# Performance work log

Hardware: AMD Instinct MI355X
Metric: run time of the kernel (lower is better)

Reference implementation:

```python
import jax, jax.numpy as jnp
import numpy as np

SPATIAL_SHAPES = [(128, 128), (64, 64), (32, 32), (16, 16)]  # sum HW = 21760
N_HEADS, N_LEVELS, N_POINTS, EMBED = 8, 4, 4, 256
HEAD_D = EMBED // N_HEADS
B, NQ = 2, 10000
NV = sum(h * w for h, w in SPATIAL_SHAPES)


def setup_inputs() -> dict:
    key = jax.random.key(0)
    ks = jax.random.split(key, 12)
    s = 0.02
    return {
        "query": jax.random.normal(ks[0], (B, NQ, EMBED), jnp.float32),
        "key": jax.random.normal(ks[1], (B, NV, EMBED), jnp.float32),
        "value": jax.random.normal(ks[2], (B, NV, EMBED), jnp.float32),
        "W_off": jax.random.normal(ks[3], (EMBED, N_HEADS * N_LEVELS * N_POINTS * 2), jnp.float32) * s,
        "b_off": jax.random.uniform(ks[4], (N_HEADS * N_LEVELS * N_POINTS * 2,), jnp.float32, -0.9, 0.9),
        "W_attn": jax.random.normal(ks[5], (EMBED, N_HEADS * N_LEVELS * N_POINTS), jnp.float32) * s,
        "b_attn": jnp.zeros((N_HEADS * N_LEVELS * N_POINTS,), jnp.float32),
        "W_v": jax.random.normal(ks[6], (EMBED, EMBED), jnp.float32) * s,
        "b_v": jnp.zeros((EMBED,), jnp.float32),
        "W_out": jax.random.normal(ks[7], (EMBED, EMBED), jnp.float32) * s,
        "b_out": jnp.zeros((EMBED,), jnp.float32),
    }


def bilinear_sample(img, gx, gy):
    """img: [N, Hs, Ws, C]; gx, gy: [N, P] in [-1, 1].
    Torch grid_sample semantics: bilinear, align_corners=True, padding_mode='zeros'.
    gx indexes width, gy indexes height."""
    N, Hs, Ws, C = img.shape
    px = (gx + 1.0) * 0.5 * (Ws - 1)
    py = (gy + 1.0) * 0.5 * (Hs - 1)
    x0 = jnp.floor(px)
    y0 = jnp.floor(py)
    wx = (px - x0)[..., None]
    wy = (py - y0)[..., None]
    x0i = x0.astype(jnp.int32)
    y0i = y0.astype(jnp.int32)
    flat = img.reshape(N, Hs * Ws, C)

    def gather(xi, yi):
        valid = ((xi >= 0) & (xi < Ws) & (yi >= 0) & (yi < Hs))[..., None]
        xc = jnp.clip(xi, 0, Ws - 1)
        yc = jnp.clip(yi, 0, Hs - 1)
        idx = yc * Ws + xc  # [N, P]
        v = jnp.take_along_axis(flat, idx[..., None], axis=1)  # [N, P, C]
        return jnp.where(valid, v, 0.0)

    v00 = gather(x0i, y0i)
    v01 = gather(x0i + 1, y0i)
    v10 = gather(x0i, y0i + 1)
    v11 = gather(x0i + 1, y0i + 1)
    top = v00 * (1.0 - wx) + v01 * wx
    bot = v10 * (1.0 - wx) + v11 * wx
    return top * (1.0 - wy) + bot * wy


def reference(query, key, value, W_off, b_off, W_attn, b_attn, W_v, b_v, W_out, b_out):
    Bq, Nq, _ = query.shape
    # value projection -> per-head values
    v = (value @ W_v + b_v).reshape(Bq, NV, N_HEADS, HEAD_D)
    # sampling locations (used directly as normalized [-1,1] grid coords) and weights
    off = (query @ W_off + b_off).reshape(Bq, Nq, N_HEADS, N_LEVELS, N_POINTS, 2)
    attn = (query @ W_attn + b_attn).reshape(Bq, Nq, N_HEADS, N_LEVELS, N_POINTS)
    attn = jax.nn.softmax(attn, axis=-1)  # softmax over points per level (as in source)

    out = jnp.zeros((Bq, Nq, EMBED), query.dtype)
    start = 0
    for lvl, (Hs, Ws) in enumerate(SPATIAL_SHAPES):
        vl = v[:, start:start + Hs * Ws].reshape(Bq, Hs, Ws, N_HEADS, HEAD_D)
        start += Hs * Ws
        vl = vl.transpose(0, 3, 1, 2, 4).reshape(Bq * N_HEADS, Hs, Ws, HEAD_D)
        gl = off[:, :, :, lvl]  # [B, Nq, H, P, 2]
        gl = gl.transpose(0, 2, 1, 3, 4).reshape(Bq * N_HEADS, Nq * N_POINTS, 2)
        samp = bilinear_sample(vl, gl[..., 0], gl[..., 1])  # [B*H, Nq*P, D]
        samp = samp.reshape(Bq, N_HEADS, Nq, N_POINTS, HEAD_D)
        wl = attn[:, :, :, lvl].transpose(0, 2, 1, 3)  # [B, H, Nq, P]
        out = out + jnp.einsum('bhqp,bhqpd->bqhd', wl, samp).reshape(Bq, Nq, EMBED)
    return out @ W_out + b_out
```

## Files before the change

### kernel.cpp

```cpp
#include <hip/hip_runtime.h>
#include <math.h>

#define B_   2
#define NQ_  10000
#define NV_  21760
#define EMB  256
#define MQ   (B_*NQ_)
#define MV   (B_*NV_)

typedef short bf16x8 __attribute__((ext_vector_type(8)));
typedef float f32x4  __attribute__((ext_vector_type(4)));

__device__ constexpr int LSc[4] = {0, 16384, 20480, 21504};

__device__ __forceinline__ unsigned short f2bf(float x) {
  unsigned u = __builtin_bit_cast(unsigned, x);
  u += 0x7FFFu + ((u >> 16) & 1u);
  return (unsigned short)(u >> 16);
}
__device__ __forceinline__ float bf2f(unsigned short s) {
  return __builtin_bit_cast(float, (unsigned)s << 16);
}

__global__ __launch_bounds__(256) void prep_weights(
    const float* __restrict__ Wv, const float* __restrict__ Wattn,
    const float* __restrict__ Woff, const float* __restrict__ Wout,
    unsigned short* __restrict__ WvT, unsigned short* __restrict__ WoutT,
    unsigned short* __restrict__ WqHi, unsigned short* __restrict__ WqLo) {
  int n = blockIdx.x;
  int k = threadIdx.x;
  if (n < 256) {
    WvT[n * 256 + k] = f2bf(Wv[k * 256 + n]);
  } else if (n < 512) {
    int c = n - 256;
    WoutT[c * 256 + k] = f2bf(Wout[k * 256 + c]);
  } else {
    int qr = n - 512;
    float x = (qr < 256) ? Woff[k * 256 + qr] : Wattn[k * 128 + (qr - 256)];
    unsigned short hi = f2bf(x);
    WqHi[qr * 256 + k] = hi;
    WqLo[qr * 256 + k] = f2bf(x - bf2f(hi));
  }
}

template <int MODE, typename OutT, bool VPERM = false>
__global__ __launch_bounds__(256) void gemm_mfma(
    const void* __restrict__ Aa,
    const unsigned short* __restrict__ Bt, const unsigned short* __restrict__ Bt2,
    const float* __restrict__ bias, const float* __restrict__ bias2,
    OutT* __restrict__ C, float* __restrict__ C2, int M, int N) {
  constexpr int BM = 128, BK = 32;
  __shared__ unsigned short As[(MODE == 3 ? 2 : 1) * BM * BK];
  __shared__ unsigned short Bs[(MODE == 3 ? 2 : 1) * BM * BK];
  unsigned short* As2 = As + BM * BK;
  unsigned short* Bs2 = Bs + BM * BK;

  const int tid = threadIdx.x;
  const int lane = tid & 63, wv = tid >> 6;
  const int wr = wv >> 1, wc = wv & 1;
  const int row0 = blockIdx.x * BM, col0 = blockIdx.y * BM;

  auto lds_addr = [](int row, int kslot) -> int {
    return row * 64 + ((kslot ^ ((row >> 1) & 3)) << 4);
  };

  auto stage_bf = [&](unsigned short* dst, const unsigned short* src,
                      int rbase, int rmax, int kk) {
#pragma unroll
    for (int i = 0; i < 2; ++i) {
      int idx = tid + 256 * i;
      int row = idx >> 2, ks = idx & 3;
      int rg = min(rbase + row, rmax);
      bf16x8 vdat = *(const bf16x8*)(src + (size_t)rg * 256 + kk + ks * 8);
      *(bf16x8*)((char*)dst + lds_addr(row, ks)) = vdat;
    }
  };
  auto stage_cvt = [&](unsigned short* dst, const float* src,
                       int rbase, int rmax, int kk) {
#pragma unroll
    for (int i = 0; i < 4; ++i) {
      int idx = tid + 256 * i;
      int row = idx >> 3, c4 = idx & 7;
      int rg = min(rbase + row, rmax);
      float4 vdat = *(const float4*)(src + (size_t)rg * 256 + kk + c4 * 4);
      ushort4 o;
      o.x = f2bf(vdat.x); o.y = f2bf(vdat.y);
      o.z = f2bf(vdat.z); o.w = f2bf(vdat.w);
      *(ushort4*)((char*)dst + lds_addr(row, c4 >> 1) + (c4 & 1) * 8) = o;
    }
  };
  auto stage_cvt2 = [&](unsigned short* dstH, unsigned short* dstL,
                        const float* src, int rbase, int rmax, int kk) {
#pragma unroll
    for (int i = 0; i < 4; ++i) {
      int idx = tid + 256 * i;
      int row = idx >> 3, c4 = idx & 7;
      int rg = min(rbase + row, rmax);
      float4 vdat = *(const float4*)(src + (size_t)rg * 256 + kk + c4 * 4);
      ushort4 hh, ll;
      hh.x = f2bf(vdat.x); ll.x = f2bf(vdat.x - bf2f(hh.x));
      hh.y = f2bf(vdat.y); ll.y = f2bf(vdat.y - bf2f(hh.y));
      hh.z = f2bf(vdat.z); ll.z = f2bf(vdat.z - bf2f(hh.z));
      hh.w = f2bf(vdat.w); ll.w = f2bf(vdat.w - bf2f(hh.w));
      int a = lds_addr(row, c4 >> 1) + (c4 & 1) * 8;
      *(ushort4*)((char*)dstH + a) = hh;
      *(ushort4*)((char*)dstL + a) = ll;
    }
  };

  const bool three_term = (MODE == 3) && (col0 < 256);

  f32x4 acc[4][4] = {};

  for (int kk = 0; kk < 256; kk += BK) {
    if (kk) __syncthreads();
    if constexpr (MODE == 1)
      stage_cvt(As, (const float*)Aa, row0, M - 1, kk);
    else if constexpr (MODE == 3) {
      if (three_term)
        stage_cvt2(As, As2, (const float*)Aa, row0, M - 1, kk);
      else
        stage_cvt(As, (const float*)Aa, row0, M - 1, kk);
    } else
      stage_bf(As, (const unsigned short*)Aa, row0, M - 1, kk);
    stage_bf(Bs, Bt, col0, N - 1, kk);
    if constexpr (MODE == 3)
      if (three_term) stage_bf(Bs2, Bt2, col0, N - 1, kk);
    __syncthreads();

    const int kslot = lane >> 4;
    bf16x8 af[4], bfr[4];
#pragma unroll
    for (int i = 0; i < 4; ++i) {
      int ra = wr * 64 + i * 16 + (lane & 15);
      af[i] = *(const bf16x8*)((const char*)As + lds_addr(ra, kslot));
      int rb = wc * 64 + i * 16 + (lane & 15);
      bfr[i] = *(const bf16x8*)((const char*)Bs + lds_addr(rb, kslot));
    }
#pragma unroll
    for (int mi = 0; mi < 4; ++mi)
#pragma unroll
      for (int ni = 0; ni < 4; ++ni)
        acc[mi][ni] = __builtin_amdgcn_mfma_f32_16x16x32_bf16(
            af[mi], bfr[ni], acc[mi][ni], 0, 0, 0);

    if constexpr (MODE == 3) {
      if (three_term) {
        bf16x8 af2[4], bfr2[4];
#pragma unroll
        for (int i = 0; i < 4; ++i) {
          int ra = wr * 64 + i * 16 + (lane & 15);
          af2[i] = *(const bf16x8*)((const char*)As2 + lds_addr(ra, kslot));
          int rb = wc * 64 + i * 16 + (lane & 15);
          bfr2[i] = *(const bf16x8*)((const char*)Bs2 + lds_addr(rb, kslot));
        }
#pragma unroll
        for (int mi = 0; mi < 4; ++mi)
#pragma unroll
          for (int ni = 0; ni < 4; ++ni) {
            acc[mi][ni] = __builtin_amdgcn_mfma_f32_16x16x32_bf16(
                af2[mi], bfr[ni], acc[mi][ni], 0, 0, 0);
            acc[mi][ni] = __builtin_amdgcn_mfma_f32_16x16x32_bf16(
                af[mi], bfr2[ni], acc[mi][ni], 0, 0, 0);
          }
      }
    }
  }

  if constexpr (VPERM) {
    float bb4[4];
#pragma unroll
    for (int ni = 0; ni < 4; ++ni)
      bb4[ni] = bias[col0 + wc * 64 + ni * 16 + (lane & 15)];
#pragma unroll
    for (int mi = 0; mi < 4; ++mi) {
#pragma unroll
      for (int r = 0; r < 4; ++r) {
        int row = row0 + wr * 64 + mi * 16 + ((lane >> 4) << 2) + r;
        int pix = row, bb2 = 0;
        if (pix >= NV_) { bb2 = 1; pix -= NV_; }
        int lvl = (pix >= 16384) + (pix >= 20480) + (pix >= 21504);
        int sh = 7 - lvl;
        int rel = pix - LSc[lvl];
        int x = rel & ((1 << sh) - 1), y = rel >> sh;
        unsigned pairoff = ((unsigned)((y << (sh - 1)) + (x >> 1)) << 10) |
                           ((unsigned)(x & 1) << 3);
        char* vout = (char*)C + ((size_t)bb2 * NV_ + LSc[lvl]) * 512 + pairoff;
#pragma unroll
        for (int ni = 0; ni < 4; ++ni) {
          int gcol = col0 + wc * 64 + ni * 16 + (lane & 15);
          float val = acc[mi][ni][r] + bb4[ni];
          int h = gcol >> 5, d = gcol & 31;
          *(unsigned short*)(vout + h * 128 + (d >> 2) * 16 + (d & 3) * 2) =
              f2bf(val);
        }
      }
    }
  } else {
#pragma unroll
    for (int ni = 0; ni < 4; ++ni) {
      int gcol = col0 + wc * 64 + ni * 16 + (lane & 15);
      float bb = (MODE == 3 && gcol >= 256) ? bias2[gcol - 256] : bias[gcol];
#pragma unroll
      for (int mi = 0; mi < 4; ++mi) {
        int rowbase = row0 + wr * 64 + mi * 16 + ((lane >> 4) << 2);
        f32x4 a = acc[mi][ni];
#pragma unroll
        for (int r = 0; r < 4; ++r) {
          int row = rowbase + r;
          if (row < M) {
            float val = a[r] + bb;
            if constexpr (MODE == 3) {
              if (gcol >= 256)
                C2[(size_t)row * 128 + (gcol - 256)] = val;
              else
                C[(size_t)row * 256 + gcol] = (OutT)val;
            } else if constexpr (sizeof(OutT) == 2) {
              C[(size_t)row * N + gcol] = (OutT)f2bf(val);
            } else {
              C[(size_t)row * N + gcol] = (OutT)val;
            }
          }
        }
      }
    }
  }
}

__global__ __launch_bounds__(256) void msda_sample6(
    const char* __restrict__ v,
    const float* __restrict__ off,
    const float* __restrict__ attnlg,
    ushort4* __restrict__ tmp4) {
  __shared__ unsigned coeff[4 * 136 * 8];
  const int lane = threadIdx.x & 63;
  const int wq = threadIdx.x >> 6;
  const int bq = blockIdx.x * 4 + wq;
  const int b = (blockIdx.x * 4) / NQ_;

  unsigned* cbase = coeff + wq * (136 * 8);
  const float* offq = off + (size_t)bq * 256;
  const float* attq = attnlg + (size_t)bq * 128;

#pragma unroll
  for (int i = 0; i < 2; ++i) {
    int c = lane + i * 64;
    int h = c >> 4, l = (c >> 2) & 3, p = c & 3;
    int Wl = 128 >> l, sh = 7 - l;

    const float* lg = attq + h * 16 + l * 4;
    float l0 = lg[0], l1 = lg[1], l2 = lg[2], l3 = lg[3];
    float m = fmaxf(fmaxf(l0, l1), fmaxf(l2, l3));
    float e0 = expf(l0 - m), e1 = expf(l1 - m);
    float e2 = expf(l2 - m), e3 = expf(l3 - m);
    float ep = (p == 0) ? e0 : (p == 1) ? e1 : (p == 2) ? e2 : e3;
    float wsm = ep / (e0 + e1 + e2 + e3);

    float gx = offq[h * 32 + (l * 4 + p) * 2 + 0];
    float gy = offq[h * 32 + (l * 4 + p) * 2 + 1];
    float s = 0.5f * (float)(Wl - 1);
    float px = fmaf(gx, s, s), py = fmaf(gy, s, s);
    float x0f = floorf(px), y0f = floorf(py);
    float wx = px - x0f, wy = py - y0f;
    int x0 = (int)x0f, y0 = (int)y0f;

    bool bx0 = (unsigned)x0 < (unsigned)Wl, bx1 = (unsigned)(x0 + 1) < (unsigned)Wl;
    bool by0 = (unsigned)y0 < (unsigned)Wl, by1 = (unsigned)(y0 + 1) < (unsigned)Wl;
    int x0c = min(max(x0, 0), Wl - 1), x1c = min(max(x0 + 1, 0), Wl - 1);
    int y0c = min(max(y0, 0), Wl - 1), y1c = min(max(y0 + 1, 0), Wl - 1);

    auto poff = [&](int xx, int yy) -> unsigned {
      return ((unsigned)((yy << (sh - 1)) + (xx >> 1)) << 10) |
             ((unsigned)(xx & 1) << 3);
    };

    float wxm = 1.f - wx, wym = 1.f - wy;
    float w00 = (bx0 & by0) ? wsm * wxm * wym : 0.f;
    float w01 = (bx1 & by0) ? wsm * wx  * wym : 0.f;
    float w10 = (bx0 & by1) ? wsm * wxm * wy  : 0.f;
    float w11 = (bx1 & by1) ? wsm * wx  * wy  : 0.f;

    unsigned* slot = cbase + (c + h) * 8;
    uint4 s0;
    s0.x = poff(x0c, y0c);
    s0.y = poff(x1c, y0c);
    s0.z = poff(x0c, y1c);
    s0.w = poff(x1c, y1c);
    *(uint4*)slot = s0;
    uint4 s1;
    s1.x = __builtin_bit_cast(unsigned, w00);
    s1.y = __builtin_bit_cast(unsigned, w01);
    s1.z = __builtin_bit_cast(unsigned, w10);
    s1.w = __builtin_bit_cast(unsigned, w11);
    *(uint4*)(slot + 4) = s1;
  }
  __syncthreads();

  const int h = lane >> 3, c4 = lane & 7;
  const unsigned laneoff = (unsigned)(h * 128 + c4 * 16);
  float4 acc = make_float4(0.f, 0.f, 0.f, 0.f);

#pragma unroll
  for (int l = 0; l < 4; ++l) {
    const char* lb = v + ((size_t)b * NV_ + LSc[l]) * 512;
    const unsigned* cb = cbase + (h * 17 + l * 4) * 8;
#pragma unroll
    for (int p = 0; p < 4; ++p) {
      uint4 s0 = *(const uint4*)(cb + p * 8);
      uint4 s1 = *(const uint4*)(cb + p * 8 + 4);
      float w00 = __builtin_bit_cast(float, s1.x);
      float w01 = __builtin_bit_cast(float, s1.y);
      float w10 = __builtin_bit_cast(float, s1.z);
      float w11 = __builtin_bit_cast(float, s1.w);

      uint2 r00 = *(const uint2*)(lb + (laneoff + s0.x));
      uint2 r01 = *(const uint2*)(lb + (laneoff + s0.y));
      uint2 r10 = *(const uint2*)(lb + (laneoff + s0.z));
      uint2 r11 = *(const uint2*)(lb + (laneoff + s0.w));

      acc.x += w00 * __builtin_bit_cast(float, r00.x << 16)
             + w01 * __builtin_bit_cast(float, r01.x << 16)
             + w10 * __builtin_bit_cast(float, r10.x << 16)
             + w11 * __builtin_bit_cast(float, r11.x << 16);
      acc.y += w00 * __builtin_bit_cast(float, r00.x & 0xFFFF0000u)
             + w01 * __builtin_bit_cast(float, r01.x & 0xFFFF0000u)
             + w10 * __builtin_bit_cast(float, r10.x & 0xFFFF0000u)
             + w11 * __builtin_bit_cast(float, r11.x & 0xFFFF0000u);
      acc.z += w00 * __builtin_bit_cast(float, r00.y << 16)
             + w01 * __builtin_bit_cast(float, r01.y << 16)
             + w10 * __builtin_bit_cast(float, r10.y << 16)
             + w11 * __builtin_bit_cast(float, r11.y << 16);
      acc.w += w00 * __builtin_bit_cast(float, r00.y & 0xFFFF0000u)
             + w01 * __builtin_bit_cast(float, r01.y & 0xFFFF0000u)
             + w10 * __builtin_bit_cast(float, r10.y & 0xFFFF0000u)
             + w11 * __builtin_bit_cast(float, r11.y & 0xFFFF0000u);
    }
  }
  ushort4 o;
  o.x = f2bf(acc.x); o.y = f2bf(acc.y); o.z = f2bf(acc.z); o.w = f2bf(acc.w);
  tmp4[(size_t)bq * 64 + lane] = o;
}

extern "C" void kernel_launch(void* const* d_in, const int* in_sizes, int n_in,
                              void* d_out, int out_size, void* d_ws, size_t ws_size,
                              hipStream_t stream) {
  const float* query  = (const float*)d_in[0];
  const float* value  = (const float*)d_in[2];
  const float* W_off  = (const float*)d_in[3];
  const float* b_off  = (const float*)d_in[4];
  const float* W_attn = (const float*)d_in[5];
  const float* b_attn = (const float*)d_in[6];
  const float* W_v    = (const float*)d_in[7];
  const float* b_v    = (const float*)d_in[8];
  const float* W_out  = (const float*)d_in[9];
  const float* b_out  = (const float*)d_in[10];
  float* out = (float*)d_out;

  char* p = (char*)d_ws;
  unsigned short* v_bf  = (unsigned short*)p; p += (size_t)MV * 256 * 2;
  float*          off_w = (float*)p;          p += (size_t)MQ * 256 * 4;
  float*          att_w = (float*)p;          p += (size_t)MQ * 128 * 4;
  unsigned short* tmp_bf= (unsigned short*)p; p += (size_t)MQ * 256 * 2;
  unsigned short* WvT   = (unsigned short*)p; p += 256 * 256 * 2;
  unsigned short* WoutT = (unsigned short*)p; p += 256 * 256 * 2;
  unsigned short* WqHi  = (unsigned short*)p; p += 384 * 256 * 2;
  unsigned short* WqLo  = (unsigned short*)p; p += 384 * 256 * 2;

  dim3 blk(256);

  prep_weights<<<dim3(896), blk, 0, stream>>>(
      W_v, W_attn, W_off, W_out, WvT, WoutT, WqHi, WqLo);

  gemm_mfma<1, unsigned short, true><<<dim3(MV / 128, 2), blk, 0, stream>>>(
      value, WvT, nullptr, b_v, nullptr, v_bf, nullptr, MV, 256);

  gemm_mfma<3, float><<<dim3((MQ + 127) / 128, 3), blk, 0, stream>>>(
      query, WqHi, WqLo, b_off, b_attn, off_w, att_w, MQ, 384);

  msda_sample6<<<dim3(MQ / 4), blk, 0, stream>>>(
      (const char*)v_bf, off_w, att_w, (ushort4*)tmp_bf);

  gemm_mfma<0, float><<<dim3((MQ + 127) / 128, 2), blk, 0, stream>>>(
      tmp_bf, WoutT, nullptr, b_out, nullptr, out, nullptr, MQ, 256);
}
```

Baseline: 125.5 us.

## Merge value and query projection GEMMs into one launch; split sampling levels across waves

The value-projection and query-projection GEMMs now run in a single kernel. Block IDs are interleaved so that both GEMMs' tiles share the GPU at once instead of running back to back. The sampling kernel now uses 512 threads, with two waves per query each handling two of the four levels, and adds an LDS reduction to combine the partial sums. This aims to raise parallelism and latency hiding in the gather-bound sampler and to remove a launch gap, at the cost of extra barriers, an LDS round trip, and higher shared-memory use in the merged GEMM.

Measured after the change: 141.4 us. 12.7% more time.

```diff
diff --git a/kernel.cpp b/kernel.cpp
--- a/kernel.cpp
+++ b/kernel.cpp
@@ -43,22 +43,21 @@
   }
 }
 
-template <int MODE, typename OutT, bool VPERM = false>
-__global__ __launch_bounds__(256) void gemm_mfma(
+template <int MODE, typename OutT, bool VPERM>
+__device__ __forceinline__ void gemm_body(
     const void* __restrict__ Aa,
     const unsigned short* __restrict__ Bt, const unsigned short* __restrict__ Bt2,
     const float* __restrict__ bias, const float* __restrict__ bias2,
-    OutT* __restrict__ C, float* __restrict__ C2, int M, int N) {
+    OutT* __restrict__ C, float* __restrict__ C2, int M, int N,
+    int bx, int by, unsigned short* As, unsigned short* Bs) {
   constexpr int BM = 128, BK = 32;
-  __shared__ unsigned short As[(MODE == 3 ? 2 : 1) * BM * BK];
-  __shared__ unsigned short Bs[(MODE == 3 ? 2 : 1) * BM * BK];
   unsigned short* As2 = As + BM * BK;
   unsigned short* Bs2 = Bs + BM * BK;
 
   const int tid = threadIdx.x;
   const int lane = tid & 63, wv = tid >> 6;
   const int wr = wv >> 1, wc = wv & 1;
-  const int row0 = blockIdx.x * BM, col0 = blockIdx.y * BM;
+  const int row0 = bx * BM, col0 = by * BM;
 
   auto lds_addr = [](int row, int kslot) -> int {
     return row * 64 + ((kslot ^ ((row >> 1) & 3)) << 4);
@@ -227,14 +226,50 @@
   }
 }
 
-__global__ __launch_bounds__(256) void msda_sample6(
+__global__ __launch_bounds__(256) void gemm_projs(
+    const float* __restrict__ value, const unsigned short* __restrict__ WvT,
+    const float* __restrict__ b_v, unsigned short* __restrict__ v_bf,
+    const float* __restrict__ query, const unsigned short* __restrict__ WqHi,
+    const unsigned short* __restrict__ WqLo, const float* __restrict__ b_off,
+    const float* __restrict__ b_attn, float* __restrict__ off_w,
+    float* __restrict__ att_w) {
+  __shared__ unsigned short smem[4 * 128 * 32];
+  int id = blockIdx.x;
+  int vidx = -1, qidx = -1;
+  if (id < 942) { if (id & 1) qidx = id >> 1; else vidx = id >> 1; }
+  else vidx = 471 + (id - 942);
+  if (vidx >= 0) {
+    gemm_body<1, unsigned short, true>(
+        value, WvT, nullptr, b_v, nullptr, v_bf, nullptr, MV, 256,
+        vidx % 340, vidx / 340, smem, smem + 4096);
+  } else {
+    gemm_body<3, float, false>(
+        query, WqHi, WqLo, b_off, b_attn, off_w, att_w, MQ, 384,
+        qidx % 157, qidx / 157, smem, smem + 8192);
+  }
+}
+
+__global__ __launch_bounds__(256) void gemm_out(
+    const unsigned short* __restrict__ tmp_bf,
+    const unsigned short* __restrict__ WoutT, const float* __restrict__ b_out,
+    float* __restrict__ out) {
+  __shared__ unsigned short smem[2 * 128 * 32];
+  gemm_body<0, float, false>(
+      tmp_bf, WoutT, nullptr, b_out, nullptr, out, nullptr, MQ, 256,
+      blockIdx.x, blockIdx.y, smem, smem + 4096);
+}
+
+__global__ __launch_bounds__(512) void msda_sample7(
     const char* __restrict__ v,
     const float* __restrict__ off,
     const float* __restrict__ attnlg,
     ushort4* __restrict__ tmp4) {
   __shared__ unsigned coeff[4 * 136 * 8];
-  const int lane = threadIdx.x & 63;
-  const int wq = threadIdx.x >> 6;
+  const int tid = threadIdx.x;
+  const int lane = tid & 63;
+  const int wid = tid >> 6;
+  const int wq = wid >> 1;
+  const int w = wid & 1;
   const int bq = blockIdx.x * 4 + wq;
   const int b = (blockIdx.x * 4) / NQ_;
 
@@ -242,10 +277,9 @@
   const float* offq = off + (size_t)bq * 256;
   const float* attq = attnlg + (size_t)bq * 128;
 
-#pragma unroll
-  for (int i = 0; i < 2; ++i) {
-    int c = lane + i * 64;
-    int h = c >> 4, l = (c >> 2) & 3, p = c & 3;
+  {
+    int h = lane >> 3, dl = (lane >> 2) & 1, p = lane & 3;
+    int l = 2 * w + dl;
     int Wl = 128 >> l, sh = 7 - l;
 
     const float* lg = attq + h * 16 + l * 4;
@@ -280,7 +314,7 @@
     float w10 = (bx0 & by1) ? wsm * wxm * wy  : 0.f;
     float w11 = (bx1 & by1) ? wsm * wx  * wy  : 0.f;
 
-    unsigned* slot = cbase + (c + h) * 8;
+    unsigned* slot = cbase + (h * 17 + l * 4 + p) * 8;
     uint4 s0;
     s0.x = poff(x0c, y0c);
     s0.y = poff(x1c, y0c);
@@ -301,7 +335,8 @@
   float4 acc = make_float4(0.f, 0.f, 0.f, 0.f);
 
 #pragma unroll
-  for (int l = 0; l < 4; ++l) {
+  for (int dl = 0; dl < 2; ++dl) {
+    const int l = 2 * w + dl;
     const char* lb = v + ((size_t)b * NV_ + LSc[l]) * 512;
     const unsigned* cb = cbase + (h * 17 + l * 4) * 8;
 #pragma unroll
@@ -336,9 +371,18 @@
              + w11 * __builtin_bit_cast(float, r11.y & 0xFFFF0000u);
     }
   }
-  ushort4 o;
-  o.x = f2bf(acc.x); o.y = f2bf(acc.y); o.z = f2bf(acc.z); o.w = f2bf(acc.w);
-  tmp4[(size_t)bq * 64 + lane] = o;
+
+  __syncthreads();
+  float4* red = (float4*)coeff;
+  if (w == 1) red[wq * 64 + lane] = acc;
+  __syncthreads();
+  if (w == 0) {
+    float4 o2 = red[wq * 64 + lane];
+    acc.x += o2.x; acc.y += o2.y; acc.z += o2.z; acc.w += o2.w;
+    ushort4 o;
+    o.x = f2bf(acc.x); o.y = f2bf(acc.y); o.z = f2bf(acc.z); o.w = f2bf(acc.w);
+    tmp4[(size_t)bq * 64 + lane] = o;
+  }
 }
 
 extern "C" void kernel_launch(void* const* d_in, const int* in_sizes, int n_in,
@@ -366,20 +410,15 @@
   unsigned short* WqHi  = (unsigned short*)p; p += 384 * 256 * 2;
   unsigned short* WqLo  = (unsigned short*)p; p += 384 * 256 * 2;
 
-  dim3 blk(256);
-
-  prep_weights<<<dim3(896), blk, 0, stream>>>(
+  prep_weights<<<dim3(896), dim3(256), 0, stream>>>(
       W_v, W_attn, W_off, W_out, WvT, WoutT, WqHi, WqLo);
 
-  gemm_mfma<1, unsigned short, true><<<dim3(MV / 128, 2), blk, 0, stream>>>(
-      value, WvT, nullptr, b_v, nullptr, v_bf, nullptr, MV, 256);
-
-  gemm_mfma<3, float><<<dim3((MQ + 127) / 128, 3), blk, 0, stream>>>(
-      query, WqHi, WqLo, b_off, b_attn, off_w, att_w, MQ, 384);
-
-  msda_sample6<<<dim3(MQ / 4), blk, 0, stream>>>(
+  gemm_projs<<<dim3(1151), dim3(256), 0, stream>>>(
+      value, WvT, b_v, v_bf, query, WqHi, WqLo, b_off, b_attn, off_w, att_w);
+
+  msda_sample7<<<dim3(MQ / 4), dim3(512), 0, stream>>>(
       (const char*)v_bf, off_w, att_w, (ushort4*)tmp_bf);
 
-  gemm_mfma<0, float><<<dim3((MQ + 127) / 128, 2), blk, 0, stream>>>(
-      tmp_bf, WoutT, nullptr, b_out, nullptr, out, nullptr, MQ, 256);
-}
+  gemm_out<<<dim3((MQ + 127) / 128, 2), dim3(256), 0, stream>>>(
+      tmp_bf, WoutT, b_out, out);
+}
```

## Split sampling levels across two waves per query with LDS reduction

Applied to the files above, without the earlier changes.

The sampling kernel now uses 512 threads per block, with two wavefronts per query. Each wave handles two of the four pyramid levels, both for computing coefficients and for the gather-accumulate. The partial sums are combined through shared memory before the bf16 store. This doubles the number of waves available to hide gather latency and halves the serial loop per wave. The cost is an extra barrier, an LDS round trip and more threads per block.

Measured after the change: 125.3 us. Within noise of the previous version (-0.2%).

```diff
diff --git a/kernel.cpp b/kernel.cpp
--- a/kernel.cpp
+++ b/kernel.cpp
@@ -227,14 +227,17 @@
   }
 }
 
-__global__ __launch_bounds__(256) void msda_sample6(
+__global__ __launch_bounds__(512) void msda_sample7(
     const char* __restrict__ v,
     const float* __restrict__ off,
     const float* __restrict__ attnlg,
     ushort4* __restrict__ tmp4) {
   __shared__ unsigned coeff[4 * 136 * 8];
-  const int lane = threadIdx.x & 63;
-  const int wq = threadIdx.x >> 6;
+  const int tid = threadIdx.x;
+  const int lane = tid & 63;
+  const int wid = tid >> 6;
+  const int wq = wid >> 1;
+  const int w = wid & 1;
   const int bq = blockIdx.x * 4 + wq;
   const int b = (blockIdx.x * 4) / NQ_;
 
@@ -242,10 +245,9 @@
   const float* offq = off + (size_t)bq * 256;
   const float* attq = attnlg + (size_t)bq * 128;
 
-#pragma unroll
-  for (int i = 0; i < 2; ++i) {
-    int c = lane + i * 64;
-    int h = c >> 4, l = (c >> 2) & 3, p = c & 3;
+  {
+    int h = lane >> 3, dl = (lane >> 2) & 1, p = lane & 3;
+    int l = 2 * w + dl;
     int Wl = 128 >> l, sh = 7 - l;
 
     const float* lg = attq + h * 16 + l * 4;
@@ -280,7 +282,7 @@
     float w10 = (bx0 & by1) ? wsm * wxm * wy  : 0.f;
     float w11 = (bx1 & by1) ? wsm * wx  * wy  : 0.f;
 
-    unsigned* slot = cbase + (c + h) * 8;
+    unsigned* slot = cbase + (h * 17 + l * 4 + p) * 8;
     uint4 s0;
     s0.x = poff(x0c, y0c);
     s0.y = poff(x1c, y0c);
@@ -301,7 +303,8 @@
   float4 acc = make_float4(0.f, 0.f, 0.f, 0.f);
 
 #pragma unroll
-  for (int l = 0; l < 4; ++l) {
+  for (int dl = 0; dl < 2; ++dl) {
+    const int l = 2 * w + dl;
     const char* lb = v + ((size_t)b * NV_ + LSc[l]) * 512;
     const unsigned* cb = cbase + (h * 17 + l * 4) * 8;
 #pragma unroll
@@ -336,9 +339,18 @@
              + w11 * __builtin_bit_cast(float, r11.y & 0xFFFF0000u);
     }
   }
-  ushort4 o;
-  o.x = f2bf(acc.x); o.y = f2bf(acc.y); o.z = f2bf(acc.z); o.w = f2bf(acc.w);
-  tmp4[(size_t)bq * 64 + lane] = o;
+
+  __syncthreads();
+  float4* red = (float4*)coeff;
+  if (w == 1) red[wq * 64 + lane] = acc;
+  __syncthreads();
+  if (w == 0) {
+    float4 o2 = red[wq * 64 + lane];
+    acc.x += o2.x; acc.y += o2.y; acc.z += o2.z; acc.w += o2.w;
+    ushort4 o;
+    o.x = f2bf(acc.x); o.y = f2bf(acc.y); o.z = f2bf(acc.z); o.w = f2bf(acc.w);
+    tmp4[(size_t)bq * 64 + lane] = o;
+  }
 }
 
 extern "C" void kernel_launch(void* const* d_in, const int* in_sizes, int n_in,
@@ -366,20 +378,18 @@
   unsigned short* WqHi  = (unsigned short*)p; p += 384 * 256 * 2;
   unsigned short* WqLo  = (unsigned short*)p; p += 384 * 256 * 2;
 
-  dim3 blk(256);
-
-  prep_weights<<<dim3(896), blk, 0, stream>>>(
+  prep_weights<<<dim3(896), dim3(256), 0, stream>>>(
       W_v, W_attn, W_off, W_out, WvT, WoutT, WqHi, WqLo);
 
-  gemm_mfma<1, unsigned short, true><<<dim3(MV / 128, 2), blk, 0, stream>>>(
+  gemm_mfma<1, unsigned short, true><<<dim3(MV / 128, 2), dim3(256), 0, stream>>>(
       value, WvT, nullptr, b_v, nullptr, v_bf, nullptr, MV, 256);
 
-  gemm_mfma<3, float><<<dim3((MQ + 127) / 128, 3), blk, 0, stream>>>(
+  gemm_mfma<3, float><<<dim3((MQ + 127) / 128, 3), dim3(256), 0, stream>>>(
       query, WqHi, WqLo, b_off, b_attn, off_w, att_w, MQ, 384);
 
-  msda_sample6<<<dim3(MQ / 4), blk, 0, stream>>>(
+  msda_sample7<<<dim3(MQ / 4), dim3(512), 0, stream>>>(
       (const char*)v_bf, off_w, att_w, (ushort4*)tmp_bf);
 
-  gemm_mfma<0, float><<<dim3((MQ + 127) / 128, 2), blk, 0, stream>>>(
+  gemm_mfma<0, float><<<dim3((MQ + 127) / 128, 2), dim3(256), 0, stream>>>(
       tmp_bf, WoutT, nullptr, b_out, nullptr, out, nullptr, MQ, 256);
 }
```
